# Kernel optimization log

Measured on AMD Instinct MI355X. Metric: run time of the kernel, lower is better.

The kernel has to match this reference:

```python
import jax, jax.numpy as jnp
import numpy as np

D_MODEL = 1024
N_HEAD = 16
D_QKV = 64
B, L = 2, 2048
LN_EPS = 1e-5


def setup_inputs() -> dict:
    key = jax.random.key(0)
    ks = jax.random.split(key, 5)
    # xavier-normal-ish scale for [H, d_model, d_qkv] params
    std_in = (2.0 / (D_MODEL + D_QKV)) ** 0.5
    return {
        "x": jax.random.normal(ks[0], (B, L, D_MODEL), jnp.float32),
        "w_q": jax.random.normal(ks[1], (N_HEAD, D_MODEL, D_QKV), jnp.float32) * std_in,
        "w_k": jax.random.normal(ks[2], (N_HEAD, D_MODEL, D_QKV), jnp.float32) * std_in,
        "w_v": jax.random.normal(ks[3], (N_HEAD, D_MODEL, D_QKV), jnp.float32) * std_in,
        "w_o": jax.random.normal(ks[4], (N_HEAD, D_QKV, D_MODEL), jnp.float32) * std_in,
        "ln_gamma": jnp.ones((D_MODEL,), jnp.float32),
        "ln_beta": jnp.zeros((D_MODEL,), jnp.float32),
    }


def reference(x, w_q, w_k, w_v, w_o, ln_gamma, ln_beta):
    # q,k,v: [B, H, L, d_qkv]
    q = jnp.einsum('hmq,blm->bhlq', w_q, x)
    k = jnp.einsum('hmq,blm->bhlq', w_k, x)
    v = jnp.einsum('hmq,blm->bhlq', w_v, x)
    # scores: [B, H, L, L]
    s = jnp.einsum('bhiq,bhjq->bhij', q, k) / (D_QKV ** 0.5)
    s = jax.nn.softmax(s, axis=-1)
    # (dropout disabled: eval-mode reference)
    att = jnp.einsum('bhij,bhjq->bhiq', s, v)          # [B, H, L, d_qkv]
    out = jnp.einsum('bhlq,hqm->blm', att, w_o)        # [B, L, d_model]
    y = x + out                                        # residual
    mu = jnp.mean(y, axis=-1, keepdims=True)
    var = jnp.var(y, axis=-1, keepdims=True)
    return (y - mu) * jax.lax.rsqrt(var + LN_EPS) * ln_gamma + ln_beta
```

## Files before the change

### kernel.cpp

```cpp
#include <hip/hip_runtime.h>
#include <hip/hip_bf16.h>
#include <cstdint>

#define B_      2
#define L_      2048
#define DM_     1024
#define H_      16
#define DQ_     64
#define LN_EPS  1e-5f
#define QSCALE  0.1803368801111204f

typedef unsigned short u16;
typedef unsigned int   u32;
typedef __attribute__((ext_vector_type(8)))  short short8;
typedef __attribute__((ext_vector_type(4)))  unsigned short u16x4;
typedef __attribute__((ext_vector_type(4)))  float f32x4;
typedef __attribute__((ext_vector_type(16))) float f32x16;

__device__ __forceinline__ u16 f2b(float f) {
  __hip_bfloat16 h = __float2bfloat16(f);
  return *reinterpret_cast<u16*>(&h);
}

__device__ __forceinline__ void gl_lds16(const void* g, void* l) {
  auto gp = reinterpret_cast<const __attribute__((address_space(1))) unsigned int*>(
      reinterpret_cast<uintptr_t>(g));
  auto lp = reinterpret_cast<__attribute__((address_space(3))) unsigned int*>(
      reinterpret_cast<uintptr_t>(l));
  __builtin_amdgcn_global_load_lds(gp, lp, 16, 0, 0);
}

__device__ __forceinline__ short8 frag8(const u16* base, int row, int lchunk) {
  return *(const short8*)(base + row * 64 + ((lchunk ^ (row & 7)) << 3));
}

__global__ __launch_bounds__(256) void cast_x(const float* __restrict__ x,
                                              u16* __restrict__ xb) {
  int i = blockIdx.x * 256 + threadIdx.x;
  float4 v = ((const float4*)x)[i];
  u16x4 o = { f2b(v.x), f2b(v.y), f2b(v.z), f2b(v.w) };
  *(u16x4*)(xb + (size_t)i * 4) = o;
}

__global__ __launch_bounds__(256) void cast_wqkv(const float* __restrict__ wq,
    const float* __restrict__ wk, const float* __restrict__ wv, u16* __restrict__ wt) {
  const int mt = blockIdx.x, h = blockIdx.y, wh = blockIdx.z;
  const float* in = ((wh == 0) ? wq : (wh == 1) ? wk : wv) + (size_t)h * DM_ * DQ_;
  __shared__ float Ls[64][65];
  const int t = threadIdx.x;
  #pragma unroll
  for (int i = 0; i < 16; ++i) {
    int idx = i * 256 + t, r = idx >> 6, c = idx & 63;
    Ls[r][c] = in[(size_t)(mt * 64 + r) * DQ_ + c];
  }
  __syncthreads();
  u16* outb = wt + (size_t)(wh * H_ + h) * DQ_ * DM_;
  #pragma unroll
  for (int i = 0; i < 16; ++i) {
    int idx = i * 256 + t, q = idx >> 6, mm = idx & 63;
    outb[(size_t)q * DM_ + mt * 64 + mm] = f2b(Ls[mm][q]);
  }
}

__global__ __launch_bounds__(256) void cast_wo(const float* __restrict__ wo,
                                               u16* __restrict__ wot) {
  const int mt = blockIdx.x, kt = blockIdx.y;
  __shared__ float Ls[64][65];
  const int t = threadIdx.x;
  #pragma unroll
  for (int i = 0; i < 16; ++i) {
    int idx = i * 256 + t, r = idx >> 6, c = idx & 63;
    Ls[r][c] = wo[(size_t)(kt * 64 + r) * DM_ + mt * 64 + c];
  }
  __syncthreads();
  #pragma unroll
  for (int i = 0; i < 16; ++i) {
    int idx = i * 256 + t, mm = idx >> 6, kk = idx & 63;
    wot[(size_t)(mt * 64 + mm) * DM_ + kt * 64 + kk] = f2b(Ls[kk][mm]);
  }
}

__global__ __launch_bounds__(256) void qkv_big(const u16* __restrict__ xb,
    const u16* __restrict__ wt, u16* __restrict__ Q, u16* __restrict__ K,
    u16* __restrict__ Vtg) {
  const int nt = blockIdx.x, mt = blockIdx.y;
  __shared__ __align__(16) u16 As_[128 * 64];
  __shared__ __align__(16) u16 Bs_[128 * 64];
  const int t = threadIdx.x, w = t >> 6, lane = t & 63;
  const int lx = lane & 15, lq = lane >> 4;
  const int row0 = mt * 128, n0 = nt * 128;
  const int r8 = lane >> 3, lc = (lane & 7) ^ r8;

  const u16* gA = xb + (size_t)(row0 + w * 32 + r8) * DM_ + lc * 8;
  const u16* gB = wt + (size_t)(n0  + w * 32 + r8) * DM_ + lc * 8;
  u16* lA = As_ + (w * 32) * 64;
  u16* lB = Bs_ + (w * 32) * 64;

  f32x4 z = {0.f, 0.f, 0.f, 0.f};
  f32x4 acc[2][8];
  #pragma unroll
  for (int mb = 0; mb < 2; ++mb)
    #pragma unroll
    for (int nb = 0; nb < 8; ++nb) acc[mb][nb] = z;

  for (int k0 = 0; k0 < DM_; k0 += 64) {
    #pragma unroll
    for (int i = 0; i < 4; ++i) {
      gl_lds16(gA + (size_t)i * 8 * DM_ + k0, lA + i * 8 * 64);
      gl_lds16(gB + (size_t)i * 8 * DM_ + k0, lB + i * 8 * 64);
    }
    __syncthreads();
    short8 af[2][2];
    #pragma unroll
    for (int mb = 0; mb < 2; ++mb)
      #pragma unroll
      for (int kh = 0; kh < 2; ++kh)
        af[mb][kh] = frag8(As_, w * 32 + mb * 16 + lx, (kh << 2) | lq);
    #pragma unroll
    for (int nb = 0; nb < 8; ++nb) {
      short8 b0 = frag8(Bs_, nb * 16 + lx, lq);
      short8 b1 = frag8(Bs_, nb * 16 + lx, 4 | lq);
      acc[0][nb] = __builtin_amdgcn_mfma_f32_16x16x32_bf16(af[0][0], b0, acc[0][nb], 0, 0, 0);
      acc[0][nb] = __builtin_amdgcn_mfma_f32_16x16x32_bf16(af[0][1], b1, acc[0][nb], 0, 0, 0);
      acc[1][nb] = __builtin_amdgcn_mfma_f32_16x16x32_bf16(af[1][0], b0, acc[1][nb], 0, 0, 0);
      acc[1][nb] = __builtin_amdgcn_mfma_f32_16x16x32_bf16(af[1][1], b1, acc[1][nb], 0, 0, 0);
    }
    __syncthreads();
  }
  const int wh = n0 >> 10;
  const float oscale = (wh == 0) ? QSCALE : 1.0f;
  u16* qk = (wh == 0) ? Q : K;
  #pragma unroll
  for (int mb = 0; mb < 2; ++mb)
    #pragma unroll
    for (int nb = 0; nb < 8; ++nb)
      #pragma unroll
      for (int r = 0; r < 4; ++r) {
        int row = row0 + w * 32 + mb * 16 + lq * 4 + r;
        int bb = row >> 11, l = row & 2047;
        int n = n0 + nb * 16 + lx;
        int hd = n & 1023, hh = hd >> 6, d = hd & 63;
        u16 val = f2b(acc[mb][nb][r] * oscale);
        if (wh == 2)
          Vtg[((size_t)(bb * H_ + hh) * DQ_ + d) * L_ + l] = val;
        else
          qk[((size_t)(bb * H_ + hh) * L_ + l) * DQ_ + d] = val;
      }
}

__global__ __launch_bounds__(256) void attn_mfma(const u16* __restrict__ Q,
    const u16* __restrict__ K, const u16* __restrict__ Vtg, u16* __restrict__ att) {
  const int qt = blockIdx.x, h = blockIdx.y, b = blockIdx.z;
  __shared__ __align__(16) u16 Qs_[128 * 64];
  __shared__ __align__(16) u16 Ks_[64 * 64];
  __shared__ __align__(16) u16 Vt_[64 * 64];
  __shared__ __align__(16) u16 Ps[4][32][72];
  const int t = threadIdx.x, w = t >> 6, lane = t & 63;
  const int c = lane & 31, lsel = lane >> 5;
  const int r8 = lane >> 3, lc = (lane & 7) ^ r8;
  const size_t bh  = (size_t)(b * H_ + h) * L_ * DQ_;
  const size_t bhv = (size_t)(b * H_ + h) * DQ_ * L_;

  const u16* gQ = Q + bh + (size_t)(qt * 128 + w * 32 + r8) * DQ_ + lc * 8;
  #pragma unroll
  for (int i = 0; i < 4; ++i) gl_lds16(gQ + (size_t)i * 8 * DQ_, Qs_ + (w * 32 + i * 8) * 64);
  __syncthreads();
  short8 qb[4];
  #pragma unroll
  for (int km = 0; km < 4; ++km) qb[km] = frag8(Qs_, w * 32 + c, (km << 1) | lsel);

  const u16* gK = K   + bh  + (size_t)(w * 16 + r8) * DQ_ + lc * 8;
  const u16* gV = Vtg + bhv + (size_t)(w * 16 + r8) * L_  + lc * 8;
  u16* lK = Ks_ + (w * 16) * 64;
  u16* lV = Vt_ + (w * 16) * 64;

  f32x16 zz = {0.f,0.f,0.f,0.f,0.f,0.f,0.f,0.f,0.f,0.f,0.f,0.f,0.f,0.f,0.f,0.f};
  f32x16 oacc0 = zz, oacc1 = zz, lacc = zz;
  const short one_bf = (short)0x3F80;
  short8 ones = {one_bf, one_bf, one_bf, one_bf, one_bf, one_bf, one_bf, one_bf};

  for (int kt = 0; kt < L_ / 64; ++kt) {
    __syncthreads();
    #pragma unroll
    for (int i = 0; i < 2; ++i) {
      gl_lds16(gK + (size_t)(kt * 64 + i * 8) * DQ_, lK + i * 8 * 64);
      gl_lds16(gV + (size_t)i * 8 * L_ + kt * 64,    lV + i * 8 * 64);
    }
    __syncthreads();

    #pragma unroll
    for (int kb = 0; kb < 2; ++kb) {
      f32x16 s = zz;
      #pragma unroll
      for (int km = 0; km < 4; ++km) {
        short8 ka = frag8(Ks_, kb * 32 + c, (km << 1) | lsel);
        s = __builtin_amdgcn_mfma_f32_32x32x16_bf16(ka, qb[km], s, 0, 0, 0);
      }
      #pragma unroll
      for (int g = 0; g < 4; ++g) {
        float p0 = __builtin_amdgcn_exp2f(s[4 * g + 0]);
        float p1 = __builtin_amdgcn_exp2f(s[4 * g + 1]);
        float p2 = __builtin_amdgcn_exp2f(s[4 * g + 2]);
        float p3 = __builtin_amdgcn_exp2f(s[4 * g + 3]);
        uint2 pv;
        pv.x = __builtin_amdgcn_perm(__float_as_uint(p1), __float_as_uint(p0), 0x07060302u);
        pv.y = __builtin_amdgcn_perm(__float_as_uint(p3), __float_as_uint(p2), 0x07060302u);
        *(uint2*)&Ps[w][c][kb * 32 + g * 8 + lsel * 4] = pv;
      }
    }
    __syncthreads();

    #pragma unroll
    for (int km = 0; km < 4; ++km) {
      short8 pa  = *(const short8*)&Ps[w][c][km * 16 + lsel * 8];
      short8 vb0 = frag8(Vt_, c,      (km << 1) | lsel);
      short8 vb1 = frag8(Vt_, 32 + c, (km << 1) | lsel);
      oacc0 = __builtin_amdgcn_mfma_f32_32x32x16_bf16(pa, vb0, oacc0, 0, 0, 0);
      oacc1 = __builtin_amdgcn_mfma_f32_32x32x16_bf16(pa, vb1, oacc1, 0, 0, 0);
      lacc  = __builtin_amdgcn_mfma_f32_32x32x16_bf16(pa, ones, lacc, 0, 0, 0);
    }
  }

  const int qrow_base = qt * 128 + w * 32;
  #pragma unroll
  for (int r = 0; r < 16; ++r) {
    int qr = (r & 3) + 8 * (r >> 2) + 4 * lsel;
    float inv = 1.0f / lacc[r];
    size_t base = (size_t)(b * L_ + qrow_base + qr) * DM_ + h * DQ_;
    att[base + c]      = f2b(oacc0[r] * inv);
    att[base + 32 + c] = f2b(oacc1[r] * inv);
  }
}

__global__ __launch_bounds__(256) void oproj_big(const u16* __restrict__ A,
    const u16* __restrict__ wot, float* __restrict__ out) {
  const int nt = blockIdx.x, mt = blockIdx.y;
  __shared__ __align__(16) u16 As_[128 * 64];
  __shared__ __align__(16) u16 Bs_[64 * 64];
  const int t = threadIdx.x, w = t >> 6, lane = t & 63;
  const int lx = lane & 15, lq = lane >> 4;
  const int row0 = mt * 128, n0 = nt * 64;
  const int r8 = lane >> 3, lc = (lane & 7) ^ r8;

  const u16* gA = A   + (size_t)(row0 + w * 32 + r8) * DM_ + lc * 8;
  const u16* gB = wot + (size_t)(n0  + w * 16 + r8) * DM_ + lc * 8;
  u16* lA = As_ + (w * 32) * 64;
  u16* lB = Bs_ + (w * 16) * 64;

  f32x4 z = {0.f, 0.f, 0.f, 0.f};
  f32x4 acc[2][4];
  #pragma unroll
  for (int mb = 0; mb < 2; ++mb)
    #pragma unroll
    for (int nb = 0; nb < 4; ++nb) acc[mb][nb] = z;

  for (int k0 = 0; k0 < DM_; k0 += 64) {
    #pragma unroll
    for (int i = 0; i < 4; ++i)
      gl_lds16(gA + (size_t)i * 8 * DM_ + k0, lA + i * 8 * 64);
    #pragma unroll
    for (int i = 0; i < 2; ++i)
      gl_lds16(gB + (size_t)i * 8 * DM_ + k0, lB + i * 8 * 64);
    __syncthreads();
    short8 af[2][2];
    #pragma unroll
    for (int mb = 0; mb < 2; ++mb)
      #pragma unroll
      for (int kh = 0; kh < 2; ++kh)
        af[mb][kh] = frag8(As_, w * 32 + mb * 16 + lx, (kh << 2) | lq);
    #pragma unroll
    for (int nb = 0; nb < 4; ++nb) {
      short8 b0 = frag8(Bs_, nb * 16 + lx, lq);
      short8 b1 = frag8(Bs_, nb * 16 + lx, 4 | lq);
      acc[0][nb] = __builtin_amdgcn_mfma_f32_16x16x32_bf16(af[0][0], b0, acc[0][nb], 0, 0, 0);
      acc[0][nb] = __builtin_amdgcn_mfma_f32_16x16x32_bf16(af[0][1], b1, acc[0][nb], 0, 0, 0);
      acc[1][nb] = __builtin_amdgcn_mfma_f32_16x16x32_bf16(af[1][0], b0, acc[1][nb], 0, 0, 0);
      acc[1][nb] = __builtin_amdgcn_mfma_f32_16x16x32_bf16(af[1][1], b1, acc[1][nb], 0, 0, 0);
    }
    __syncthreads();
  }
  #pragma unroll
  for (int mb = 0; mb < 2; ++mb)
    #pragma unroll
    for (int nb = 0; nb < 4; ++nb)
      #pragma unroll
      for (int r = 0; r < 4; ++r) {
        int row = row0 + w * 32 + mb * 16 + lq * 4 + r;
        out[(size_t)row * DM_ + n0 + nb * 16 + lx] = acc[mb][nb][r];
      }
}

__global__ __launch_bounds__(256) void resid_ln(
    const float* __restrict__ x, const float* __restrict__ gamma,
    const float* __restrict__ beta, float* __restrict__ out) {
  const int row = blockIdx.x;
  const int t   = threadIdx.x;
  const float4* xp = (const float4*)(x   + (size_t)row * DM_);
  float4*       yp = (float4*)      (out + (size_t)row * DM_);

  float4 xv = xp[t];
  float4 av = yp[t];
  float y0 = xv.x + av.x, y1 = xv.y + av.y, y2 = xv.z + av.z, y3 = xv.w + av.w;

  float s  = y0 + y1 + y2 + y3;
  float s2 = y0 * y0 + y1 * y1 + y2 * y2 + y3 * y3;
  #pragma unroll
  for (int off = 32; off > 0; off >>= 1) {
    s  += __shfl_xor(s,  off, 64);
    s2 += __shfl_xor(s2, off, 64);
  }
  __shared__ float red[8];
  const int wave = t >> 6, lane = t & 63;
  if (lane == 0) { red[wave] = s; red[4 + wave] = s2; }
  __syncthreads();
  s  = red[0] + red[1] + red[2] + red[3];
  s2 = red[4] + red[5] + red[6] + red[7];

  const float mean = s * (1.f / DM_);
  const float var  = s2 * (1.f / DM_) - mean * mean;
  const float inv  = rsqrtf(var + LN_EPS);

  const float4 g  = ((const float4*)gamma)[t];
  const float4 bt = ((const float4*)beta)[t];
  float4 r;
  r.x = (y0 - mean) * inv * g.x + bt.x;
  r.y = (y1 - mean) * inv * g.y + bt.y;
  r.z = (y2 - mean) * inv * g.z + bt.z;
  r.w = (y3 - mean) * inv * g.w + bt.w;
  yp[t] = r;
}

extern "C" void kernel_launch(void* const* d_in, const int* in_sizes, int n_in,
                              void* d_out, int out_size, void* d_ws, size_t ws_size,
                              hipStream_t stream) {
  const float* x     = (const float*)d_in[0];
  const float* wq    = (const float*)d_in[1];
  const float* wk    = (const float*)d_in[2];
  const float* wv    = (const float*)d_in[3];
  const float* wo    = (const float*)d_in[4];
  const float* gamma = (const float*)d_in[5];
  const float* beta  = (const float*)d_in[6];
  float* out = (float*)d_out;

  char* ws = (char*)d_ws;
  u16* xb  = (u16*)ws;
  u16* Qb  = (u16*)(ws + ((size_t)8  << 20));
  u16* Kb  = (u16*)(ws + ((size_t)16 << 20));
  u16* Vtg = (u16*)(ws + ((size_t)24 << 20));
  u16* wt  = (u16*)(ws + ((size_t)32 << 20));
  u16* wot = (u16*)(ws + ((size_t)38 << 20));
  u16* att = (u16*)(ws + ((size_t)40 << 20));

  cast_x   <<<4096, 256, 0, stream>>>(x, xb);
  cast_wqkv<<<dim3(16, 16, 3), 256, 0, stream>>>(wq, wk, wv, wt);
  cast_wo  <<<dim3(16, 16),    256, 0, stream>>>(wo, wot);
  qkv_big  <<<dim3(24, 32),    256, 0, stream>>>(xb, wt, Qb, Kb, Vtg);
  attn_mfma<<<dim3(L_ / 128, H_, B_), 256, 0, stream>>>(Qb, Kb, Vtg, att);
  oproj_big<<<dim3(16, 32),    256, 0, stream>>>(att, wot, out);
  resid_ln <<<B_ * L_, 256, 0, stream>>>(x, gamma, beta, out);
}
```

Measured before the change: 202.0 us.

## Double-buffer K/V tiles in attention and merge the cast kernels into one launch

```diff
diff --git a/kernel.cpp b/kernel.cpp
--- a/kernel.cpp
+++ b/kernel.cpp
@@ -34,49 +34,49 @@
   return *(const short8*)(base + row * 64 + ((lchunk ^ (row & 7)) << 3));
 }
 
-__global__ __launch_bounds__(256) void cast_x(const float* __restrict__ x,
-                                              u16* __restrict__ xb) {
-  int i = blockIdx.x * 256 + threadIdx.x;
-  float4 v = ((const float4*)x)[i];
-  u16x4 o = { f2b(v.x), f2b(v.y), f2b(v.z), f2b(v.w) };
-  *(u16x4*)(xb + (size_t)i * 4) = o;
-}
-
-__global__ __launch_bounds__(256) void cast_wqkv(const float* __restrict__ wq,
-    const float* __restrict__ wk, const float* __restrict__ wv, u16* __restrict__ wt) {
-  const int mt = blockIdx.x, h = blockIdx.y, wh = blockIdx.z;
-  const float* in = ((wh == 0) ? wq : (wh == 1) ? wk : wv) + (size_t)h * DM_ * DQ_;
+__global__ __launch_bounds__(256) void prep_all(
+    const float* __restrict__ x, const float* __restrict__ wq,
+    const float* __restrict__ wk, const float* __restrict__ wv,
+    const float* __restrict__ wo, u16* __restrict__ xb,
+    u16* __restrict__ wt, u16* __restrict__ wot) {
   __shared__ float Ls[64][65];
   const int t = threadIdx.x;
-  #pragma unroll
-  for (int i = 0; i < 16; ++i) {
-    int idx = i * 256 + t, r = idx >> 6, c = idx & 63;
-    Ls[r][c] = in[(size_t)(mt * 64 + r) * DQ_ + c];
-  }
-  __syncthreads();
-  u16* outb = wt + (size_t)(wh * H_ + h) * DQ_ * DM_;
-  #pragma unroll
-  for (int i = 0; i < 16; ++i) {
-    int idx = i * 256 + t, q = idx >> 6, mm = idx & 63;
-    outb[(size_t)q * DM_ + mt * 64 + mm] = f2b(Ls[mm][q]);
-  }
-}
-
-__global__ __launch_bounds__(256) void cast_wo(const float* __restrict__ wo,
-                                               u16* __restrict__ wot) {
-  const int mt = blockIdx.x, kt = blockIdx.y;
-  __shared__ float Ls[64][65];
-  const int t = threadIdx.x;
-  #pragma unroll
-  for (int i = 0; i < 16; ++i) {
-    int idx = i * 256 + t, r = idx >> 6, c = idx & 63;
-    Ls[r][c] = wo[(size_t)(kt * 64 + r) * DM_ + mt * 64 + c];
-  }
-  __syncthreads();
-  #pragma unroll
-  for (int i = 0; i < 16; ++i) {
-    int idx = i * 256 + t, mm = idx >> 6, kk = idx & 63;
-    wot[(size_t)(mt * 64 + mm) * DM_ + kt * 64 + kk] = f2b(Ls[kk][mm]);
+  const int bx = blockIdx.x;
+  if (bx < 4096) {
+    int i = bx * 256 + t;
+    float4 v = ((const float4*)x)[i];
+    u16x4 o = { f2b(v.x), f2b(v.y), f2b(v.z), f2b(v.w) };
+    *(u16x4*)(xb + (size_t)i * 4) = o;
+  } else if (bx < 4096 + 768) {
+    int b2 = bx - 4096;
+    int mt = b2 & 15, h = (b2 >> 4) & 15, wh = b2 >> 8;
+    const float* in = ((wh == 0) ? wq : (wh == 1) ? wk : wv) + (size_t)h * DM_ * DQ_;
+    #pragma unroll
+    for (int i = 0; i < 16; ++i) {
+      int idx = i * 256 + t, r = idx >> 6, c = idx & 63;
+      Ls[r][c] = in[(size_t)(mt * 64 + r) * DQ_ + c];
+    }
+    __syncthreads();
+    u16* outb = wt + (size_t)(wh * H_ + h) * DQ_ * DM_;
+    #pragma unroll
+    for (int i = 0; i < 16; ++i) {
+      int idx = i * 256 + t, q = idx >> 6, mm = idx & 63;
+      outb[(size_t)q * DM_ + mt * 64 + mm] = f2b(Ls[mm][q]);
+    }
+  } else {
+    int b3 = bx - 4864;
+    int mt = b3 & 15, kt = b3 >> 4;
+    #pragma unroll
+    for (int i = 0; i < 16; ++i) {
+      int idx = i * 256 + t, r = idx >> 6, c = idx & 63;
+      Ls[r][c] = wo[(size_t)(kt * 64 + r) * DM_ + mt * 64 + c];
+    }
+    __syncthreads();
+    #pragma unroll
+    for (int i = 0; i < 16; ++i) {
+      int idx = i * 256 + t, mm = idx >> 6, kk = idx & 63;
+      wot[(size_t)(mt * 64 + mm) * DM_ + kt * 64 + kk] = f2b(Ls[kk][mm]);
+    }
   }
 }
 
@@ -152,8 +152,8 @@
     const u16* __restrict__ K, const u16* __restrict__ Vtg, u16* __restrict__ att) {
   const int qt = blockIdx.x, h = blockIdx.y, b = blockIdx.z;
   __shared__ __align__(16) u16 Qs_[128 * 64];
-  __shared__ __align__(16) u16 Ks_[64 * 64];
-  __shared__ __align__(16) u16 Vt_[64 * 64];
+  __shared__ __align__(16) u16 Ks_[2][64 * 64];
+  __shared__ __align__(16) u16 Vt_[2][64 * 64];
   __shared__ __align__(16) u16 Ps[4][32][72];
   const int t = threadIdx.x, w = t >> 6, lane = t & 63;
   const int c = lane & 31, lsel = lane >> 5;
@@ -164,15 +164,19 @@
   const u16* gQ = Q + bh + (size_t)(qt * 128 + w * 32 + r8) * DQ_ + lc * 8;
   #pragma unroll
   for (int i = 0; i < 4; ++i) gl_lds16(gQ + (size_t)i * 8 * DQ_, Qs_ + (w * 32 + i * 8) * 64);
+
+  const u16* gK = K   + bh  + (size_t)(w * 16 + r8) * DQ_ + lc * 8;
+  const u16* gV = Vtg + bhv + (size_t)(w * 16 + r8) * L_  + lc * 8;
+
+  #pragma unroll
+  for (int i = 0; i < 2; ++i) {
+    gl_lds16(gK + (size_t)i * 8 * DQ_, Ks_[0] + (w * 16 + i * 8) * 64);
+    gl_lds16(gV + (size_t)i * 8 * L_,  Vt_[0] + (w * 16 + i * 8) * 64);
+  }
   __syncthreads();
   short8 qb[4];
   #pragma unroll
   for (int km = 0; km < 4; ++km) qb[km] = frag8(Qs_, w * 32 + c, (km << 1) | lsel);
-
-  const u16* gK = K   + bh  + (size_t)(w * 16 + r8) * DQ_ + lc * 8;
-  const u16* gV = Vtg + bhv + (size_t)(w * 16 + r8) * L_  + lc * 8;
-  u16* lK = Ks_ + (w * 16) * 64;
-  u16* lV = Vt_ + (w * 16) * 64;
 
   f32x16 zz = {0.f,0.f,0.f,0.f,0.f,0.f,0.f,0.f,0.f,0.f,0.f,0.f,0.f,0.f,0.f,0.f};
   f32x16 oacc0 = zz, oacc1 = zz, lacc = zz;
@@ -180,20 +184,24 @@
   short8 ones = {one_bf, one_bf, one_bf, one_bf, one_bf, one_bf, one_bf, one_bf};
 
   for (int kt = 0; kt < L_ / 64; ++kt) {
-    __syncthreads();
-    #pragma unroll
-    for (int i = 0; i < 2; ++i) {
-      gl_lds16(gK + (size_t)(kt * 64 + i * 8) * DQ_, lK + i * 8 * 64);
-      gl_lds16(gV + (size_t)i * 8 * L_ + kt * 64,    lV + i * 8 * 64);
-    }
-    __syncthreads();
+    const int cur = kt & 1;
+    __syncthreads();
+
+    if (kt + 1 < L_ / 64) {
+      const int nxt = 1 - cur;
+      #pragma unroll
+      for (int i = 0; i < 2; ++i) {
+        gl_lds16(gK + (size_t)((kt + 1) * 64 + i * 8) * DQ_, Ks_[nxt] + (w * 16 + i * 8) * 64);
+        gl_lds16(gV + (size_t)i * 8 * L_ + (kt + 1) * 64,    Vt_[nxt] + (w * 16 + i * 8) * 64);
+      }
+    }
 
     #pragma unroll
     for (int kb = 0; kb < 2; ++kb) {
       f32x16 s = zz;
       #pragma unroll
       for (int km = 0; km < 4; ++km) {
-        short8 ka = frag8(Ks_, kb * 32 + c, (km << 1) | lsel);
+        short8 ka = frag8(Ks_[cur], kb * 32 + c, (km << 1) | lsel);
         s = __builtin_amdgcn_mfma_f32_32x32x16_bf16(ka, qb[km], s, 0, 0, 0);
       }
       #pragma unroll
@@ -208,13 +216,12 @@
         *(uint2*)&Ps[w][c][kb * 32 + g * 8 + lsel * 4] = pv;
       }
     }
-    __syncthreads();
 
     #pragma unroll
     for (int km = 0; km < 4; ++km) {
       short8 pa  = *(const short8*)&Ps[w][c][km * 16 + lsel * 8];
-      short8 vb0 = frag8(Vt_, c,      (km << 1) | lsel);
-      short8 vb1 = frag8(Vt_, 32 + c, (km << 1) | lsel);
+      short8 vb0 = frag8(Vt_[cur], c,      (km << 1) | lsel);
+      short8 vb1 = frag8(Vt_[cur], 32 + c, (km << 1) | lsel);
       oacc0 = __builtin_amdgcn_mfma_f32_32x32x16_bf16(pa, vb0, oacc0, 0, 0, 0);
       oacc1 = __builtin_amdgcn_mfma_f32_32x32x16_bf16(pa, vb1, oacc1, 0, 0, 0);
       lacc  = __builtin_amdgcn_mfma_f32_32x32x16_bf16(pa, ones, lacc, 0, 0, 0);
@@ -351,9 +358,7 @@
   u16* wot = (u16*)(ws + ((size_t)38 << 20));
   u16* att = (u16*)(ws + ((size_t)40 << 20));
 
-  cast_x   <<<4096, 256, 0, stream>>>(x, xb);
-  cast_wqkv<<<dim3(16, 16, 3), 256, 0, stream>>>(wq, wk, wv, wt);
-  cast_wo  <<<dim3(16, 16),    256, 0, stream>>>(wo, wot);
+  prep_all <<<5120, 256, 0, stream>>>(x, wq, wk, wv, wo, xb, wt, wot);
   qkv_big  <<<dim3(24, 32),    256, 0, stream>>>(xb, wt, Qb, Kb, Vtg);
   attn_mfma<<<dim3(L_ / 128, H_, B_), 256, 0, stream>>>(Qb, Kb, Vtg, att);
   oproj_big<<<dim3(16, 32),    256, 0, stream>>>(att, wot, out);
```

After: 194.6 us. 1.04x faster.
